# Optimization experiments

Measured on AMD Instinct MI355X. Metric: run time of the kernel, lower is better.

The kernel has to match this reference:

```python
import jax, jax.numpy as jnp
import numpy as np

N = 100000
E = 500000
F_IN = 128
HID = 64
HEADS = 4
OUT = 32
NEG_SLOPE = 0.2


def _glorot(key, shape):
    fan_in, fan_out = shape[0], shape[1]
    lim = jnp.sqrt(6.0 / (fan_in + fan_out))
    return jax.random.uniform(key, shape, jnp.float32, -lim, lim)


def setup_inputs() -> dict:
    key = jax.random.key(0)
    ks = jax.random.split(key, 20)
    x = jax.random.normal(ks[0], (N, F_IN), jnp.float32)
    edge_index = jax.random.randint(ks[1], (2, E), 0, N, jnp.int64)
    edge_attr = jax.random.uniform(ks[2], (E, 1), jnp.float32)
    d1 = HEADS * HID
    params = {
        # conv1: F_IN -> HEADS x HID
        "Wl1": _glorot(ks[3], (F_IN, d1)), "bl1": jnp.zeros((d1,), jnp.float32),
        "Wr1": _glorot(ks[4], (F_IN, d1)), "br1": jnp.zeros((d1,), jnp.float32),
        "We1": _glorot(ks[5], (1, d1)),
        "att1": _glorot(ks[6], (HEADS, HID)),
        "b1": jnp.zeros((d1,), jnp.float32),
        "Wl2": _glorot(ks[7], (d1, OUT)), "bl2": jnp.zeros((OUT,), jnp.float32),
        "Wr2": _glorot(ks[8], (d1, OUT)), "br2": jnp.zeros((OUT,), jnp.float32),
        "We2": _glorot(ks[9], (1, OUT)),
        "att2": _glorot(ks[10], (1, OUT)),
        "b2": jnp.zeros((OUT,), jnp.float32),
    }
    return {"x": x, "edge_index": edge_index, "edge_attr": edge_attr, **params}


def gatv2_conv(x, src, dst, edge_attr, Wl, bl, Wr, br, We, att, bias, heads, out_ch):
    """PyG GATv2Conv (add_self_loops=False, concat=True, share_weights=False)."""
    n = x.shape[0]
    xl = (x @ Wl + bl).reshape(n, heads, out_ch)          # source transform
    xr = (x @ Wr + br).reshape(n, heads, out_ch)          # target transform
    e = (edge_attr @ We).reshape(-1, heads, out_ch)       # [E, H, C]
    m = jax.nn.leaky_relu(xl[src] + xr[dst] + e, NEG_SLOPE)  # [E, H, C]
    alpha = jnp.einsum('ehc,hc->eh', m, att)              # [E, H]
    # softmax over edges sharing the same destination node
    amax = jax.ops.segment_max(alpha, dst, num_segments=n)
    ealpha = jnp.exp(alpha - amax[dst])
    denom = jax.ops.segment_sum(ealpha, dst, num_segments=n)
    alpha = ealpha / (denom[dst] + 1e-16)
    out = jax.ops.segment_sum(xl[src] * alpha[:, :, None], dst, num_segments=n)
    return out.reshape(n, heads * out_ch) + bias


def reference(x, edge_index, edge_attr, Wl1, bl1, Wr1, br1, We1, att1, b1,
              Wl2, bl2, Wr2, br2, We2, att2, b2):
    src, dst = edge_index[0], edge_index[1]
    h = gatv2_conv(x, src, dst, edge_attr, Wl1, bl1, Wr1, br1, We1, att1, b1, HEADS, HID)
    h = jax.nn.relu(h)  # dropout is identity at inference
    out = gatv2_conv(h, src, dst, edge_attr, Wl2, bl2, Wr2, br2, We2, att2, b2, 1, OUT)
    return out
```

## Files before the change

kernel.cpp:

```cpp
#include <hip/hip_runtime.h>
#include <cstddef>
#include <cstdint>

#define F_IN 128
#define D1   256
#define HEADS 4
#define HID   64
#define OUT_C 32
#define NEG   0.2f

typedef unsigned short ushort_t;
typedef __attribute__((ext_vector_type(8))) short short8;
typedef __attribute__((ext_vector_type(4))) float f32x4;
typedef __attribute__((ext_vector_type(4))) unsigned short ushort4v;

__device__ __forceinline__ float bu2f(ushort_t u) {
  return __uint_as_float(((unsigned)u) << 16);
}
__device__ __forceinline__ ushort_t f2bu(float f) {
  unsigned u = __float_as_uint(f);
  return (ushort_t)((u + 0x7FFF + ((u >> 16) & 1)) >> 16);
}

__global__ void prep_b1_k(const float* __restrict__ Wl, const float* __restrict__ Wr,
                          const float* __restrict__ bl, const float* __restrict__ br,
                          ushort_t* __restrict__ Bt, float* __restrict__ biasc) {
  int i = blockIdx.x * blockDim.x + threadIdx.x;
  int nn = i >> 7, k = i & 127;
  float v = (nn < D1) ? Wl[(size_t)k * D1 + nn] : Wr[(size_t)k * D1 + (nn - D1)];
  Bt[(size_t)nn * F_IN + k] = f2bu(v);
  if (k == 0) biasc[nn] = (nn < D1) ? bl[nn] : br[nn - D1];
}

__global__ void prep_b2_k(const float* __restrict__ Wl, const float* __restrict__ Wr,
                          const float* __restrict__ bl, const float* __restrict__ br,
                          ushort_t* __restrict__ Bt, float* __restrict__ biasc) {
  int i = blockIdx.x * blockDim.x + threadIdx.x;
  int nn = i >> 8, k = i & 255;
  float v = (nn < OUT_C) ? Wl[(size_t)k * OUT_C + nn] : Wr[(size_t)k * OUT_C + (nn - OUT_C)];
  Bt[(size_t)nn * D1 + k] = f2bu(v);
  if (k == 0) biasc[nn] = (nn < OUT_C) ? bl[nn] : br[nn - OUT_C];
}

template <int WM, int WN, int BK, bool CVT>
__global__ void mfma_gemm(const void* __restrict__ Av, const ushort_t* __restrict__ Bt,
                          const float* __restrict__ biasc, ushort_t* __restrict__ C,
                          int M, int N, int K) {
  constexpr int BM = WM * 64, BN = WN * 64;
  constexpr int LD = BK + 8;
  constexpr int CPR = BK / 8;
  __shared__ ushort_t As[BM][LD];
  __shared__ ushort_t Bs[BN][LD];
  const int tid = threadIdx.x;
  const int wave = tid >> 6, lane = tid & 63;
  const int wm = wave % WM, wn = wave / WM;
  const int quad = lane >> 4, l16 = lane & 15;
  const int m0 = blockIdx.x * BM, n0 = blockIdx.y * BN;
  const int nth = WM * WN * 64;
  f32x4 acc[4][4] = {};
  for (int k0 = 0; k0 < K; k0 += BK) {
    for (int i = tid; i < BM * CPR; i += nth) {
      int r = i / CPR, ch = i % CPR;
      int gr = m0 + r;
      if (CVT) {
        const float* A32 = (const float*)Av;
        f32x4 v0 = {}, v1 = {};
        if (gr < M) {
          const float* p = A32 + (size_t)gr * K + k0 + ch * 8;
          v0 = *(const f32x4*)p;
          v1 = *(const f32x4*)(p + 4);
        }
        short8 o;
        o[0] = (short)f2bu(v0[0]); o[1] = (short)f2bu(v0[1]);
        o[2] = (short)f2bu(v0[2]); o[3] = (short)f2bu(v0[3]);
        o[4] = (short)f2bu(v1[0]); o[5] = (short)f2bu(v1[1]);
        o[6] = (short)f2bu(v1[2]); o[7] = (short)f2bu(v1[3]);
        *(short8*)(&As[r][ch * 8]) = o;
      } else {
        const ushort_t* A16 = (const ushort_t*)Av;
        short8 v = {};
        if (gr < M) v = *(const short8*)(A16 + (size_t)gr * K + k0 + ch * 8);
        *(short8*)(&As[r][ch * 8]) = v;
      }
    }
    for (int i = tid; i < BN * CPR; i += nth) {
      int r = i / CPR, ch = i % CPR;
      short8 v = {};
      if (n0 + r < N) v = *(const short8*)(Bt + (size_t)(n0 + r) * K + k0 + ch * 8);
      *(short8*)(&Bs[r][ch * 8]) = v;
    }
    __syncthreads();
#pragma unroll
    for (int ks = 0; ks < BK; ks += 32) {
      short8 af[4], bfr[4];
#pragma unroll
      for (int mi = 0; mi < 4; ++mi)
        af[mi] = *(const short8*)(&As[wm * 64 + mi * 16 + l16][ks + quad * 8]);
#pragma unroll
      for (int ni = 0; ni < 4; ++ni)
        bfr[ni] = *(const short8*)(&Bs[wn * 64 + ni * 16 + l16][ks + quad * 8]);
#pragma unroll
      for (int mi = 0; mi < 4; ++mi)
#pragma unroll
        for (int ni = 0; ni < 4; ++ni)
          acc[mi][ni] = __builtin_amdgcn_mfma_f32_16x16x32_bf16(af[mi], bfr[ni],
                                                                acc[mi][ni], 0, 0, 0);
    }
    __syncthreads();
  }
#pragma unroll
  for (int mi = 0; mi < 4; ++mi) {
#pragma unroll
    for (int r = 0; r < 4; ++r) {
      int grow = m0 + wm * 64 + mi * 16 + quad * 4 + r;
      if (grow >= M) continue;
#pragma unroll
      for (int ni = 0; ni < 4; ++ni) {
        int gcol = n0 + wn * 64 + ni * 16 + l16;
        C[(size_t)grow * N + gcol] = f2bu(acc[mi][ni][r] + biasc[gcol]);
      }
    }
  }
}

__global__ void hist_k(const int* __restrict__ dst, int* __restrict__ deg, int e) {
  int i = blockIdx.x * blockDim.x + threadIdx.x;
  if (i < e) atomicAdd(&deg[dst[i]], 1);
}

__global__ void scan_block_k(const int* __restrict__ deg, int* __restrict__ row_ptr,
                             int* __restrict__ bsum, int n) {
  __shared__ int s[1024];
  int i = blockIdx.x * 1024 + threadIdx.x;
  int v = (i < n) ? deg[i] : 0;
  s[threadIdx.x] = v;
  __syncthreads();
  for (int off = 1; off < 1024; off <<= 1) {
    int t = (threadIdx.x >= off) ? s[threadIdx.x - off] : 0;
    __syncthreads();
    s[threadIdx.x] += t;
    __syncthreads();
  }
  if (i < n) row_ptr[i + 1] = s[threadIdx.x];
  if (threadIdx.x == 1023) bsum[blockIdx.x] = s[1023];
}

__global__ void scan_bsum_k(int* __restrict__ bsum, int nb) {
  __shared__ int s[128];
  int v = (threadIdx.x < nb) ? bsum[threadIdx.x] : 0;
  s[threadIdx.x] = v;
  __syncthreads();
  for (int off = 1; off < 128; off <<= 1) {
    int t = (threadIdx.x >= off) ? s[threadIdx.x - off] : 0;
    __syncthreads();
    s[threadIdx.x] += t;
    __syncthreads();
  }
  if (threadIdx.x < nb) bsum[threadIdx.x] = s[threadIdx.x] - v;
}

__global__ void add_off_k(int* __restrict__ row_ptr, const int* __restrict__ bsum, int n) {
  int i = blockIdx.x * blockDim.x + threadIdx.x;
  if (i == 0) row_ptr[0] = 0;
  if (i < n) row_ptr[i + 1] += bsum[i >> 10];
}

__global__ void copy_cursor_k(const int* __restrict__ row_ptr, int* __restrict__ cursor, int n) {
  int i = blockIdx.x * blockDim.x + threadIdx.x;
  if (i < n) cursor[i] = row_ptr[i];
}

__global__ void fill_k(const int* __restrict__ src, const int* __restrict__ dst,
                       const float* __restrict__ eattr, int* __restrict__ cursor,
                       int2* __restrict__ csr, int e) {
  int i = blockIdx.x * blockDim.x + threadIdx.x;
  if (i >= e) return;
  int p = atomicAdd(&cursor[dst[i]], 1);
  csr[p] = make_int2(src[i], __float_as_int(eattr[i]));
}

__global__ void gat1_k(const int* __restrict__ row_ptr, const int2* __restrict__ csr,
                       const ushort_t* __restrict__ C1,
                       const float* __restrict__ We, const float* __restrict__ att,
                       const float* __restrict__ bias, ushort_t* __restrict__ h1, int n) {
  int node = (int)(((size_t)blockIdx.x * blockDim.x + threadIdx.x) >> 6);
  int lane = threadIdx.x & 63;
  if (node >= n) return;
  int cb = lane * 4;
  ushort4v xr4 = *(const ushort4v*)(C1 + (size_t)node * 512 + 256 + cb);
  float xrr[4], Wev[4], attv[4], acc[4] = {0.f, 0.f, 0.f, 0.f};
  float esum = 0.f;
#pragma unroll
  for (int j = 0; j < 4; ++j) {
    xrr[j] = bu2f(xr4[j]);
    Wev[j] = We[cb + j];
    attv[j] = att[cb + j];
  }
  int p = row_ptr[node], p1 = row_ptr[node + 1];
  for (; p + 4 <= p1; p += 4) {
    int2 ee[4];
#pragma unroll
    for (int u = 0; u < 4; ++u) ee[u] = csr[p + u];
    ushort4v xl4[4];
#pragma unroll
    for (int u = 0; u < 4; ++u)
      xl4[u] = *(const ushort4v*)(C1 + (size_t)ee[u].x * 512 + cb);
    float xv[4][4], v[4];
#pragma unroll
    for (int u = 0; u < 4; ++u) {
      float wgt = __int_as_float(ee[u].y);
      v[u] = 0.f;
#pragma unroll
      for (int j = 0; j < 4; ++j) {
        xv[u][j] = bu2f(xl4[u][j]);
        float m = xv[u][j] + xrr[j] + wgt * Wev[j];
        m = m > 0.f ? m : NEG * m;
        v[u] += m * attv[j];
      }
    }
#pragma unroll
    for (int u = 0; u < 4; ++u) {
      v[u] += __shfl_xor(v[u], 1, 64);
      v[u] += __shfl_xor(v[u], 2, 64);
      v[u] += __shfl_xor(v[u], 4, 64);
      v[u] += __shfl_xor(v[u], 8, 64);
    }
#pragma unroll
    for (int u = 0; u < 4; ++u) {
      float eh = __expf(v[u]);
      esum += eh;
#pragma unroll
      for (int j = 0; j < 4; ++j) acc[j] += eh * xv[u][j];
    }
  }
  for (; p < p1; ++p) {
    int2 ed = csr[p];
    float wgt = __int_as_float(ed.y);
    ushort4v xl4 = *(const ushort4v*)(C1 + (size_t)ed.x * 512 + cb);
    float xv[4], v = 0.f;
#pragma unroll
    for (int j = 0; j < 4; ++j) {
      xv[j] = bu2f(xl4[j]);
      float m = xv[j] + xrr[j] + wgt * Wev[j];
      m = m > 0.f ? m : NEG * m;
      v += m * attv[j];
    }
    v += __shfl_xor(v, 1, 64);
    v += __shfl_xor(v, 2, 64);
    v += __shfl_xor(v, 4, 64);
    v += __shfl_xor(v, 8, 64);
    float eh = __expf(v);
    esum += eh;
#pragma unroll
    for (int j = 0; j < 4; ++j) acc[j] += eh * xv[j];
  }
  float inv = 1.f / (esum + 1e-16f);
  ushort4v o;
#pragma unroll
  for (int j = 0; j < 4; ++j) {
    float t = acc[j] * inv + bias[cb + j];
    o[j] = f2bu(t > 0.f ? t : 0.f);
  }
  *(ushort4v*)(h1 + (size_t)node * D1 + cb) = o;
}

__global__ void gat2_k(const int* __restrict__ row_ptr, const int2* __restrict__ csr,
                       const ushort_t* __restrict__ C2,
                       const float* __restrict__ We, const float* __restrict__ att,
                       const float* __restrict__ bias, float* __restrict__ out, int n) {
  size_t t = (size_t)blockIdx.x * blockDim.x + threadIdx.x;
  int node = (int)(t >> 3);
  int g = (int)(t & 7);
  if (node >= n) return;
  int cb = g * 4;
  ushort4v xr4 = *(const ushort4v*)(C2 + (size_t)node * 64 + 32 + cb);
  float xrr[4], Wev[4], attv[4], acc[4] = {0.f, 0.f, 0.f, 0.f};
  float esum = 0.f;
#pragma unroll
  for (int j = 0; j < 4; ++j) {
    xrr[j] = bu2f(xr4[j]);
    Wev[j] = We[cb + j];
    attv[j] = att[cb + j];
  }
  int p = row_ptr[node], p1 = row_ptr[node + 1];
  for (; p + 4 <= p1; p += 4) {
    int2 ee[4];
#pragma unroll
    for (int u = 0; u < 4; ++u) ee[u] = csr[p + u];
    ushort4v xl4[4];
#pragma unroll
    for (int u = 0; u < 4; ++u)
      xl4[u] = *(const ushort4v*)(C2 + (size_t)ee[u].x * 64 + cb);
    float xv[4][4], v[4];
#pragma unroll
    for (int u = 0; u < 4; ++u) {
      float wgt = __int_as_float(ee[u].y);
      v[u] = 0.f;
#pragma unroll
      for (int j = 0; j < 4; ++j) {
        xv[u][j] = bu2f(xl4[u][j]);
        float m = xv[u][j] + xrr[j] + wgt * Wev[j];
        m = m > 0.f ? m : NEG * m;
        v[u] += m * attv[j];
      }
    }
#pragma unroll
    for (int u = 0; u < 4; ++u) {
      v[u] += __shfl_xor(v[u], 1, 64);
      v[u] += __shfl_xor(v[u], 2, 64);
      v[u] += __shfl_xor(v[u], 4, 64);
    }
#pragma unroll
    for (int u = 0; u < 4; ++u) {
      float eh = __expf(v[u]);
      esum += eh;
#pragma unroll
      for (int j = 0; j < 4; ++j) acc[j] += eh * xv[u][j];
    }
  }
  for (; p < p1; ++p) {
    int2 ed = csr[p];
    float wgt = __int_as_float(ed.y);
    ushort4v xl4 = *(const ushort4v*)(C2 + (size_t)ed.x * 64 + cb);
    float xv[4], v = 0.f;
#pragma unroll
    for (int j = 0; j < 4; ++j) {
      xv[j] = bu2f(xl4[j]);
      float m = xv[j] + xrr[j] + wgt * Wev[j];
      m = m > 0.f ? m : NEG * m;
      v += m * attv[j];
    }
    v += __shfl_xor(v, 1, 64);
    v += __shfl_xor(v, 2, 64);
    v += __shfl_xor(v, 4, 64);
    float eh = __expf(v);
    esum += eh;
#pragma unroll
    for (int j = 0; j < 4; ++j) acc[j] += eh * xv[j];
  }
  float inv = 1.f / (esum + 1e-16f);
  f32x4 ov;
#pragma unroll
  for (int j = 0; j < 4; ++j) ov[j] = acc[j] * inv + bias[cb + j];
  *(f32x4*)(out + (size_t)node * OUT_C + cb) = ov;
}

extern "C" void kernel_launch(void* const* d_in, const int* in_sizes, int n_in,
                              void* d_out, int out_size, void* d_ws, size_t ws_size,
                              hipStream_t stream) {
  const float* x     = (const float*)d_in[0];
  const int*   eidx  = (const int*)d_in[1];
  const float* eattr = (const float*)d_in[2];
  const float* Wl1 = (const float*)d_in[3];
  const float* bl1 = (const float*)d_in[4];
  const float* Wr1 = (const float*)d_in[5];
  const float* br1 = (const float*)d_in[6];
  const float* We1 = (const float*)d_in[7];
  const float* att1 = (const float*)d_in[8];
  const float* b1  = (const float*)d_in[9];
  const float* Wl2 = (const float*)d_in[10];
  const float* bl2 = (const float*)d_in[11];
  const float* Wr2 = (const float*)d_in[12];
  const float* br2 = (const float*)d_in[13];
  const float* We2 = (const float*)d_in[14];
  const float* att2 = (const float*)d_in[15];
  const float* b2  = (const float*)d_in[16];

  const int n = in_sizes[0] / F_IN;
  const int e = in_sizes[2];
  const int* src = eidx;
  const int* dst = eidx + e;
  float* out = (float*)d_out;

  char* w = (char*)d_ws;
  ushort_t* C1   = (ushort_t*)w;  w += (size_t)n * 512 * 2;
  ushort_t* h1b  = (ushort_t*)w;  w += (size_t)n * D1 * 2;
  ushort_t* C2   = (ushort_t*)w;  w += (size_t)n * 64 * 2;
  ushort_t* Bt1  = (ushort_t*)w;  w += 512 * F_IN * 2;
  ushort_t* Bt2  = (ushort_t*)w;  w += 64 * D1 * 2;
  float* bias1c  = (float*)w;     w += 512 * 4;
  float* bias2c  = (float*)w;     w += 64 * 4;
  int2*  csr     = (int2*)w;      w += (size_t)e * 8;
  int*   row_ptr = (int*)w;       w += ((size_t)n + 1) * 4;
  int*   cursor  = (int*)w;       w += (size_t)n * 4;
  int*   bsum    = (int*)w;       w += 512;
  int*   deg = cursor;

  dim3 blk(256);
  const int nb = (n + 1023) / 1024;

  prep_b1_k<<<(512 * 128) / 256, blk, 0, stream>>>(Wl1, Wr1, bl1, br1, Bt1, bias1c);
  prep_b2_k<<<(64 * 256) / 256, blk, 0, stream>>>(Wl2, Wr2, bl2, br2, Bt2, bias2c);

  hipMemsetAsync(deg, 0, (size_t)n * sizeof(int), stream);
  hist_k<<<(e + 255) / 256, blk, 0, stream>>>(dst, deg, e);
  scan_block_k<<<nb, 1024, 0, stream>>>(deg, row_ptr, bsum, n);
  scan_bsum_k<<<1, 128, 0, stream>>>(bsum, nb);
  add_off_k<<<(n + 255) / 256, blk, 0, stream>>>(row_ptr, bsum, n);
  copy_cursor_k<<<(n + 255) / 256, blk, 0, stream>>>(row_ptr, cursor, n);
  fill_k<<<(e + 255) / 256, blk, 0, stream>>>(src, dst, eattr, cursor, csr, e);

  mfma_gemm<2, 2, 64, true><<<dim3((n + 127) / 128, 4), blk, 0, stream>>>(
      x, Bt1, bias1c, C1, n, 512, F_IN);
  gat1_k<<<(n + 3) / 4, blk, 0, stream>>>(row_ptr, csr, C1, We1, att1, b1, h1b, n);

  mfma_gemm<2, 1, 64, false><<<dim3((n + 127) / 128, 1), dim3(128), 0, stream>>>(
      h1b, Bt2, bias2c, C2, n, 64, D1);
  gat2_k<<<((size_t)n * 8 + 255) / 256, blk, 0, stream>>>(row_ptr, csr, C2,
                                                          We2, att2, b2, out, n);
}
```

Before: 353.2 us.

## Load fp32 x once per GEMM1 row tile; widen gat1 to 8 channels per lane

```diff
diff --git a/kernel.cpp b/kernel.cpp
--- a/kernel.cpp
+++ b/kernel.cpp
@@ -13,6 +13,7 @@
 typedef __attribute__((ext_vector_type(8))) short short8;
 typedef __attribute__((ext_vector_type(4))) float f32x4;
 typedef __attribute__((ext_vector_type(4))) unsigned short ushort4v;
+typedef __attribute__((ext_vector_type(8))) unsigned short ushort8v;
 
 __device__ __forceinline__ float bu2f(ushort_t u) {
   return __uint_as_float(((unsigned)u) << 16);
@@ -42,8 +43,76 @@
   if (k == 0) biasc[nn] = (nn < OUT_C) ? bl[nn] : br[nn - OUT_C];
 }
 
-template <int WM, int WN, int BK, bool CVT>
-__global__ void mfma_gemm(const void* __restrict__ Av, const ushort_t* __restrict__ Bt,
+__global__ void gemm1_fused(const float* __restrict__ A, const ushort_t* __restrict__ Bt,
+                            const float* __restrict__ biasc, ushort_t* __restrict__ C,
+                            int M) {
+  __shared__ ushort_t As[128][136];
+  __shared__ ushort_t Bs[64][136];
+  const int tid = threadIdx.x;
+  const int wave = tid >> 6, lane = tid & 63;
+  const int wm = wave & 1, wn = wave >> 1;
+  const int quad = lane >> 4, l16 = lane & 15;
+  const int m0 = blockIdx.x * 128;
+  for (int i = tid; i < 128 * 16; i += 256) {
+    int r = i >> 4, ch = i & 15;
+    int gr = m0 + r;
+    f32x4 v0 = {}, v1 = {};
+    if (gr < M) {
+      const float* p = A + (size_t)gr * 128 + ch * 8;
+      v0 = *(const f32x4*)p;
+      v1 = *(const f32x4*)(p + 4);
+    }
+    short8 o;
+    o[0] = (short)f2bu(v0[0]); o[1] = (short)f2bu(v0[1]);
+    o[2] = (short)f2bu(v0[2]); o[3] = (short)f2bu(v0[3]);
+    o[4] = (short)f2bu(v1[0]); o[5] = (short)f2bu(v1[1]);
+    o[6] = (short)f2bu(v1[2]); o[7] = (short)f2bu(v1[3]);
+    *(short8*)(&As[r][ch * 8]) = o;
+  }
+  __syncthreads();
+  for (int nt = 0; nt < 8; ++nt) {
+    for (int i = tid; i < 64 * 16; i += 256) {
+      int r = i >> 4, ch = i & 15;
+      *(short8*)(&Bs[r][ch * 8]) =
+          *(const short8*)(Bt + ((nt * 64 + r) << 7) + ch * 8);
+    }
+    __syncthreads();
+    f32x4 acc[4][2] = {};
+#pragma unroll
+    for (int ks = 0; ks < 128; ks += 32) {
+      short8 af[4], bfr[2];
+#pragma unroll
+      for (int mi = 0; mi < 4; ++mi)
+        af[mi] = *(const short8*)(&As[wm * 64 + mi * 16 + l16][ks + quad * 8]);
+#pragma unroll
+      for (int ni = 0; ni < 2; ++ni)
+        bfr[ni] = *(const short8*)(&Bs[wn * 32 + ni * 16 + l16][ks + quad * 8]);
+#pragma unroll
+      for (int mi = 0; mi < 4; ++mi)
+#pragma unroll
+        for (int ni = 0; ni < 2; ++ni)
+          acc[mi][ni] = __builtin_amdgcn_mfma_f32_16x16x32_bf16(af[mi], bfr[ni],
+                                                                acc[mi][ni], 0, 0, 0);
+    }
+#pragma unroll
+    for (int mi = 0; mi < 4; ++mi) {
+#pragma unroll
+      for (int r = 0; r < 4; ++r) {
+        int grow = m0 + wm * 64 + mi * 16 + quad * 4 + r;
+        if (grow >= M) continue;
+#pragma unroll
+        for (int ni = 0; ni < 2; ++ni) {
+          int gcol = nt * 64 + wn * 32 + ni * 16 + l16;
+          C[(size_t)grow * 512 + gcol] = f2bu(acc[mi][ni][r] + biasc[gcol]);
+        }
+      }
+    }
+    __syncthreads();
+  }
+}
+
+template <int WM, int WN, int BK>
+__global__ void mfma_gemm(const ushort_t* __restrict__ A16, const ushort_t* __restrict__ Bt,
                           const float* __restrict__ biasc, ushort_t* __restrict__ C,
                           int M, int N, int K) {
   constexpr int BM = WM * 64, BN = WN * 64;
@@ -62,26 +131,9 @@
     for (int i = tid; i < BM * CPR; i += nth) {
       int r = i / CPR, ch = i % CPR;
       int gr = m0 + r;
-      if (CVT) {
-        const float* A32 = (const float*)Av;
-        f32x4 v0 = {}, v1 = {};
-        if (gr < M) {
-          const float* p = A32 + (size_t)gr * K + k0 + ch * 8;
-          v0 = *(const f32x4*)p;
-          v1 = *(const f32x4*)(p + 4);
-        }
-        short8 o;
-        o[0] = (short)f2bu(v0[0]); o[1] = (short)f2bu(v0[1]);
-        o[2] = (short)f2bu(v0[2]); o[3] = (short)f2bu(v0[3]);
-        o[4] = (short)f2bu(v1[0]); o[5] = (short)f2bu(v1[1]);
-        o[6] = (short)f2bu(v1[2]); o[7] = (short)f2bu(v1[3]);
-        *(short8*)(&As[r][ch * 8]) = o;
-      } else {
-        const ushort_t* A16 = (const ushort_t*)Av;
-        short8 v = {};
-        if (gr < M) v = *(const short8*)(A16 + (size_t)gr * K + k0 + ch * 8);
-        *(short8*)(&As[r][ch * 8]) = v;
-      }
+      short8 v = {};
+      if (gr < M) v = *(const short8*)(A16 + (size_t)gr * K + k0 + ch * 8);
+      *(short8*)(&As[r][ch * 8]) = v;
     }
     for (int i = tid; i < BN * CPR; i += nth) {
       int r = i / CPR, ch = i % CPR;
@@ -117,7 +169,7 @@
 #pragma unroll
       for (int ni = 0; ni < 4; ++ni) {
         int gcol = n0 + wn * 64 + ni * 16 + l16;
-        C[(size_t)grow * N + gcol] = f2bu(acc[mi][ni][r] + biasc[gcol]);
+        if (gcol < N) C[(size_t)grow * N + gcol] = f2bu(acc[mi][ni][r] + biasc[gcol]);
       }
     }
   }
@@ -159,15 +211,15 @@
   if (threadIdx.x < nb) bsum[threadIdx.x] = s[threadIdx.x] - v;
 }
 
-__global__ void add_off_k(int* __restrict__ row_ptr, const int* __restrict__ bsum, int n) {
+__global__ void add_off_k(int* __restrict__ row_ptr, const int* __restrict__ bsum,
+                          int* __restrict__ cursor, int n) {
   int i = blockIdx.x * blockDim.x + threadIdx.x;
-  if (i == 0) row_ptr[0] = 0;
-  if (i < n) row_ptr[i + 1] += bsum[i >> 10];
-}
-
-__global__ void copy_cursor_k(const int* __restrict__ row_ptr, int* __restrict__ cursor, int n) {
-  int i = blockIdx.x * blockDim.x + threadIdx.x;
-  if (i < n) cursor[i] = row_ptr[i];
+  if (i == 0) { row_ptr[0] = 0; cursor[0] = 0; }
+  if (i < n) {
+    int v = row_ptr[i + 1] + bsum[i >> 10];
+    row_ptr[i + 1] = v;
+    if (i + 1 < n) cursor[i + 1] = v;
+  }
 }
 
 __global__ void fill_k(const int* __restrict__ src, const int* __restrict__ dst,
@@ -183,85 +235,78 @@
                        const ushort_t* __restrict__ C1,
                        const float* __restrict__ We, const float* __restrict__ att,
                        const float* __restrict__ bias, ushort_t* __restrict__ h1, int n) {
-  int node = (int)(((size_t)blockIdx.x * blockDim.x + threadIdx.x) >> 6);
   int lane = threadIdx.x & 63;
+  int node = (int)((((size_t)blockIdx.x * blockDim.x + threadIdx.x)) >> 5);
   if (node >= n) return;
-  int cb = lane * 4;
-  ushort4v xr4 = *(const ushort4v*)(C1 + (size_t)node * 512 + 256 + cb);
-  float xrr[4], Wev[4], attv[4], acc[4] = {0.f, 0.f, 0.f, 0.f};
+  int cb = (lane & 31) * 8;
+  ushort8v xr8 = *(const ushort8v*)(C1 + (node << 9) + 256 + cb);
+  f32x4 w0 = *(const f32x4*)(We + cb),  w1 = *(const f32x4*)(We + cb + 4);
+  f32x4 a0 = *(const f32x4*)(att + cb), a1 = *(const f32x4*)(att + cb + 4);
+  float xrr[8], Wev[8], attv[8], acc[8];
   float esum = 0.f;
 #pragma unroll
   for (int j = 0; j < 4; ++j) {
-    xrr[j] = bu2f(xr4[j]);
-    Wev[j] = We[cb + j];
-    attv[j] = att[cb + j];
-  }
+    Wev[j] = w0[j]; Wev[j + 4] = w1[j];
+    attv[j] = a0[j]; attv[j + 4] = a1[j];
+  }
+#pragma unroll
+  for (int j = 0; j < 8; ++j) { xrr[j] = bu2f(xr8[j]); acc[j] = 0.f; }
   int p = row_ptr[node], p1 = row_ptr[node + 1];
-  for (; p + 4 <= p1; p += 4) {
-    int2 ee[4];
-#pragma unroll
-    for (int u = 0; u < 4; ++u) ee[u] = csr[p + u];
-    ushort4v xl4[4];
-#pragma unroll
-    for (int u = 0; u < 4; ++u)
-      xl4[u] = *(const ushort4v*)(C1 + (size_t)ee[u].x * 512 + cb);
-    float xv[4][4], v[4];
-#pragma unroll
-    for (int u = 0; u < 4; ++u) {
-      float wgt = __int_as_float(ee[u].y);
-      v[u] = 0.f;
-#pragma unroll
-      for (int j = 0; j < 4; ++j) {
-        xv[u][j] = bu2f(xl4[u][j]);
-        float m = xv[u][j] + xrr[j] + wgt * Wev[j];
-        m = m > 0.f ? m : NEG * m;
-        v[u] += m * attv[j];
-      }
-    }
-#pragma unroll
-    for (int u = 0; u < 4; ++u) {
-      v[u] += __shfl_xor(v[u], 1, 64);
-      v[u] += __shfl_xor(v[u], 2, 64);
-      v[u] += __shfl_xor(v[u], 4, 64);
-      v[u] += __shfl_xor(v[u], 8, 64);
-    }
-#pragma unroll
-    for (int u = 0; u < 4; ++u) {
-      float eh = __expf(v[u]);
-      esum += eh;
-#pragma unroll
-      for (int j = 0; j < 4; ++j) acc[j] += eh * xv[u][j];
-    }
-  }
-  for (; p < p1; ++p) {
-    int2 ed = csr[p];
-    float wgt = __int_as_float(ed.y);
-    ushort4v xl4 = *(const ushort4v*)(C1 + (size_t)ed.x * 512 + cb);
-    float xv[4], v = 0.f;
-#pragma unroll
-    for (int j = 0; j < 4; ++j) {
-      xv[j] = bu2f(xl4[j]);
-      float m = xv[j] + xrr[j] + wgt * Wev[j];
+  for (; p + 2 <= p1; p += 2) {
+    int2 e0 = csr[p], e1 = csr[p + 1];
+    ushort8v g0 = *(const ushort8v*)(C1 + (e0.x << 9) + cb);
+    ushort8v g1 = *(const ushort8v*)(C1 + (e1.x << 9) + cb);
+    float wg0 = __int_as_float(e0.y), wg1 = __int_as_float(e1.y);
+    float xv0[8], xv1[8], v0 = 0.f, v1 = 0.f;
+#pragma unroll
+    for (int j = 0; j < 8; ++j) {
+      xv0[j] = bu2f(g0[j]);
+      float m = xv0[j] + xrr[j] + wg0 * Wev[j];
       m = m > 0.f ? m : NEG * m;
-      v += m * attv[j];
-    }
-    v += __shfl_xor(v, 1, 64);
-    v += __shfl_xor(v, 2, 64);
-    v += __shfl_xor(v, 4, 64);
-    v += __shfl_xor(v, 8, 64);
-    float eh = __expf(v);
-    esum += eh;
-#pragma unroll
-    for (int j = 0; j < 4; ++j) acc[j] += eh * xv[j];
-  }
+      v0 += m * attv[j];
+      xv1[j] = bu2f(g1[j]);
+      float q = xv1[j] + xrr[j] + wg1 * Wev[j];
+      q = q > 0.f ? q : NEG * q;
+      v1 += q * attv[j];
+    }
+    v0 += __shfl_xor(v0, 1, 64); v1 += __shfl_xor(v1, 1, 64);
+    v0 += __shfl_xor(v0, 2, 64); v1 += __shfl_xor(v1, 2, 64);
+    v0 += __shfl_xor(v0, 4, 64); v1 += __shfl_xor(v1, 4, 64);
+    float eh0 = __expf(v0), eh1 = __expf(v1);
+    esum += eh0 + eh1;
+#pragma unroll
+    for (int j = 0; j < 8; ++j) acc[j] += eh0 * xv0[j] + eh1 * xv1[j];
+  }
+  if (p < p1) {
+    int2 e0 = csr[p];
+    ushort8v g0 = *(const ushort8v*)(C1 + (e0.x << 9) + cb);
+    float wg0 = __int_as_float(e0.y);
+    float xv0[8], v0 = 0.f;
+#pragma unroll
+    for (int j = 0; j < 8; ++j) {
+      xv0[j] = bu2f(g0[j]);
+      float m = xv0[j] + xrr[j] + wg0 * Wev[j];
+      m = m > 0.f ? m : NEG * m;
+      v0 += m * attv[j];
+    }
+    v0 += __shfl_xor(v0, 1, 64);
+    v0 += __shfl_xor(v0, 2, 64);
+    v0 += __shfl_xor(v0, 4, 64);
+    float eh0 = __expf(v0);
+    esum += eh0;
+#pragma unroll
+    for (int j = 0; j < 8; ++j) acc[j] += eh0 * xv0[j];
+  }
+  f32x4 b0 = *(const f32x4*)(bias + cb), b1 = *(const f32x4*)(bias + cb + 4);
   float inv = 1.f / (esum + 1e-16f);
-  ushort4v o;
-#pragma unroll
-  for (int j = 0; j < 4; ++j) {
-    float t = acc[j] * inv + bias[cb + j];
+  ushort8v o;
+#pragma unroll
+  for (int j = 0; j < 8; ++j) {
+    float bb = j < 4 ? b0[j] : b1[j - 4];
+    float t = acc[j] * inv + bb;
     o[j] = f2bu(t > 0.f ? t : 0.f);
   }
-  *(ushort4v*)(h1 + (size_t)node * D1 + cb) = o;
+  *(ushort8v*)(h1 + (node << 8) + cb) = o;
 }
 
 __global__ void gat2_k(const int* __restrict__ row_ptr, const int2* __restrict__ csr,
@@ -273,15 +318,13 @@
   int g = (int)(t & 7);
   if (node >= n) return;
   int cb = g * 4;
-  ushort4v xr4 = *(const ushort4v*)(C2 + (size_t)node * 64 + 32 + cb);
-  float xrr[4], Wev[4], attv[4], acc[4] = {0.f, 0.f, 0.f, 0.f};
+  ushort4v xr4 = *(const ushort4v*)(C2 + (node << 6) + 32 + cb);
+  f32x4 wv = *(const f32x4*)(We + cb);
+  f32x4 av = *(const f32x4*)(att + cb);
+  float xrr[4], acc[4] = {0.f, 0.f, 0.f, 0.f};
   float esum = 0.f;
 #pragma unroll
-  for (int j = 0; j < 4; ++j) {
-    xrr[j] = bu2f(xr4[j]);
-    Wev[j] = We[cb + j];
-    attv[j] = att[cb + j];
-  }
+  for (int j = 0; j < 4; ++j) xrr[j] = bu2f(xr4[j]);
   int p = row_ptr[node], p1 = row_ptr[node + 1];
   for (; p + 4 <= p1; p += 4) {
     int2 ee[4];
@@ -290,7 +333,7 @@
     ushort4v xl4[4];
 #pragma unroll
     for (int u = 0; u < 4; ++u)
-      xl4[u] = *(const ushort4v*)(C2 + (size_t)ee[u].x * 64 + cb);
+      xl4[u] = *(const ushort4v*)(C2 + (ee[u].x << 6) + cb);
     float xv[4][4], v[4];
 #pragma unroll
     for (int u = 0; u < 4; ++u) {
@@ -299,9 +342,9 @@
 #pragma unroll
       for (int j = 0; j < 4; ++j) {
         xv[u][j] = bu2f(xl4[u][j]);
-        float m = xv[u][j] + xrr[j] + wgt * Wev[j];
+        float m = xv[u][j] + xrr[j] + wgt * wv[j];
         m = m > 0.f ? m : NEG * m;
-        v[u] += m * attv[j];
+        v[u] += m * av[j];
       }
     }
 #pragma unroll
@@ -321,14 +364,14 @@
   for (; p < p1; ++p) {
     int2 ed = csr[p];
     float wgt = __int_as_float(ed.y);
-    ushort4v xl4 = *(const ushort4v*)(C2 + (size_t)ed.x * 64 + cb);
+    ushort4v xl4 = *(const ushort4v*)(C2 + (ed.x << 6) + cb);
     float xv[4], v = 0.f;
 #pragma unroll
     for (int j = 0; j < 4; ++j) {
       xv[j] = bu2f(xl4[j]);
-      float m = xv[j] + xrr[j] + wgt * Wev[j];
+      float m = xv[j] + xrr[j] + wgt * wv[j];
       m = m > 0.f ? m : NEG * m;
-      v += m * attv[j];
+      v += m * av[j];
     }
     v += __shfl_xor(v, 1, 64);
     v += __shfl_xor(v, 2, 64);
@@ -338,10 +381,11 @@
 #pragma unroll
     for (int j = 0; j < 4; ++j) acc[j] += eh * xv[j];
   }
+  f32x4 bv = *(const f32x4*)(bias + cb);
   float inv = 1.f / (esum + 1e-16f);
   f32x4 ov;
 #pragma unroll
-  for (int j = 0; j < 4; ++j) ov[j] = acc[j] * inv + bias[cb + j];
+  for (int j = 0; j < 4; ++j) ov[j] = acc[j] * inv + bv[j];
   *(f32x4*)(out + (size_t)node * OUT_C + cb) = ov;
 }
 
@@ -396,15 +440,14 @@
   hist_k<<<(e + 255) / 256, blk, 0, stream>>>(dst, deg, e);
   scan_block_k<<<nb, 1024, 0, stream>>>(deg, row_ptr, bsum, n);
   scan_bsum_k<<<1, 128, 0, stream>>>(bsum, nb);
-  add_off_k<<<(n + 255) / 256, blk, 0, stream>>>(row_ptr, bsum, n);
-  copy_cursor_k<<<(n + 255) / 256, blk, 0, stream>>>(row_ptr, cursor, n);
+  add_off_k<<<(n + 255) / 256, blk, 0, stream>>>(row_ptr, bsum, cursor, n);
   fill_k<<<(e + 255) / 256, blk, 0, stream>>>(src, dst, eattr, cursor, csr, e);
 
-  mfma_gemm<2, 2, 64, true><<<dim3((n + 127) / 128, 4), blk, 0, stream>>>(
-      x, Bt1, bias1c, C1, n, 512, F_IN);
-  gat1_k<<<(n + 3) / 4, blk, 0, stream>>>(row_ptr, csr, C1, We1, att1, b1, h1b, n);
-
-  mfma_gemm<2, 1, 64, false><<<dim3((n + 127) / 128, 1), dim3(128), 0, stream>>>(
+  gemm1_fused<<<(n + 127) / 128, blk, 0, stream>>>(x, Bt1, bias1c, C1, n);
+  gat1_k<<<((size_t)n * 32 + 255) / 256, blk, 0, stream>>>(row_ptr, csr, C1,
+                                                           We1, att1, b1, h1b, n);
+
+  mfma_gemm<2, 1, 64><<<dim3((n + 127) / 128, 1), dim3(128), 0, stream>>>(
       h1b, Bt2, bias2c, C2, n, 64, D1);
   gat2_k<<<((size_t)n * 8 + 255) / 256, blk, 0, stream>>>(row_ptr, csr, C2,
                                                           We2, att2, b2, out, n);
```

Measured after the change: 388.6 us. 10.0% more time.
